# Performance work log

Hardware: AMD Instinct MI355X
Metric: run time of the kernel (lower is better)

Reference implementation:

```python
import jax, jax.numpy as jnp
import numpy as np

DIM, HEADS, DH, P, C = 2048, 8, 256, 7, 128
NP = (56 // P) ** 2          # 64 patches
N = NP + 1 + NP              # 65 pos tokens concatenated with 64 patch tokens = 129
PATCH_FEAT = C * P * P       # 6272
LN_EPS = 1e-5


def patchify(x, p):
    # 'b c (h p1) (w p2) -> b (h w) (p1 p2 c)'
    b, c, H, W = x.shape
    h, w = H // p, W // p
    x = x.reshape(b, c, h, p, w, p).transpose(0, 2, 4, 3, 5, 1)
    return x.reshape(b, h * w, p * p * c)


def setup_inputs() -> dict:
    key = jax.random.key(0)
    ks = jax.random.split(key, 16)
    s = 0.02
    d = dict(
        x_q=jax.random.normal(ks[0], (64, C, 56, 56), jnp.float32),
        x_kv=jax.random.normal(ks[1], (64, C, 56, 56), jnp.float32),
        W_ex=jax.random.normal(ks[2], (PATCH_FEAT, DIM), jnp.float32) * s,
        b_ex=jnp.zeros((DIM,), jnp.float32),
        W_en=jax.random.normal(ks[3], (PATCH_FEAT, DIM), jnp.float32) * s,
        b_en=jnp.zeros((DIM,), jnp.float32),
        pos=jax.random.normal(ks[4], (1, NP + 1, DIM), jnp.float32),
        Wq=jax.random.normal(ks[5], (DIM, HEADS * DH), jnp.float32) * s,
        Wk=jax.random.normal(ks[6], (DIM, HEADS * DH), jnp.float32) * s,
        Wv=jax.random.normal(ks[7], (DIM, HEADS * DH), jnp.float32) * s,
        Wo=jax.random.normal(ks[8], (HEADS * DH, DIM), jnp.float32) * s,
        bo=jnp.zeros((DIM,), jnp.float32),
        gamma=jnp.ones((DIM,), jnp.float32),
        beta=jnp.zeros((DIM,), jnp.float32),
        Wh=jax.random.normal(ks[9], (DIM, PATCH_FEAT), jnp.float32) * s,
        bh=jnp.zeros((PATCH_FEAT,), jnp.float32),
        Wm=jax.random.normal(ks[10], (DH, N), jnp.float32) * s,
        bm=jnp.zeros((N,), jnp.float32),
    )
    return d


def reference(x_q, x_kv, W_ex, b_ex, W_en, b_en, pos, Wq, Wk, Wv, Wo, bo,
              gamma, beta, Wh, bh, Wm, bm):
    b = x_q.shape[0]
    scale = DH ** -0.5
    # image embedder: patch embed + concat pos tokens
    tq = patchify(x_q, P) @ W_ex + b_ex                      # [b, 64, DIM]
    tk = patchify(x_kv, P) @ W_en + b_en                     # [b, 64, DIM]
    posb = jnp.broadcast_to(pos, (b, NP + 1, DIM))
    tq = jnp.concatenate([posb, tq], axis=1)                 # [b, N, DIM]
    tk = jnp.concatenate([posb, tk], axis=1)                 # [b, N, DIM]

    def split_heads(t):
        return t.reshape(b, N, HEADS, DH).transpose(0, 2, 1, 3)  # b h n d

    q = split_heads(tq @ Wq)
    k = split_heads(tk @ Wk)
    v = split_heads(tk @ Wv)

    # VAE-style reparameterize: mu=k, logvar=q
    eps = jax.random.normal(jax.random.key(42), k.shape, k.dtype)
    z = k + jnp.exp(0.5 * q) * eps                           # [b, h, n, d]

    # scale + linear remap d -> N, softmax, weighted sum with v
    dots = (z * scale) @ Wm + bm                             # [b, h, n, N]
    attn = jax.nn.softmax(dots, axis=-1)
    out = jnp.einsum('bhij,bhjd->bhid', attn, v)             # [b, h, n, d]
    out = out.transpose(0, 2, 1, 3).reshape(b, N, HEADS * DH)
    out = out @ Wo + bo                                      # [b, N, DIM]

    # mlp head: LayerNorm + Linear (final rearrange-to-image is shape-only, omitted)
    mu = out.mean(-1, keepdims=True)
    var = ((out - mu) ** 2).mean(-1, keepdims=True)
    ln = (out - mu) * jax.lax.rsqrt(var + LN_EPS) * gamma + beta
    head = ln @ Wh + bh                                      # [b, N, 6272]

    qf = q.reshape(b, -1)
    kf = k.reshape(b, -1)
    qn = qf / jnp.linalg.norm(qf, axis=1, keepdims=True)
    kn = kf / jnp.linalg.norm(kf, axis=1, keepdims=True)
    return head, qn, kn
```

## Files before the change

### kernel.cpp

```cpp
#include <hip/hip_runtime.h>


typedef unsigned short u16;
typedef short bf16x8 __attribute__((ext_vector_type(8)));
typedef unsigned short u16x8 __attribute__((ext_vector_type(8)));
typedef float f32x4 __attribute__((ext_vector_type(4)));

#define WAITV(N) asm volatile("s_waitcnt vmcnt(" #N ")" ::: "memory")

static __device__ __forceinline__ void barx() {
    asm volatile("" ::: "memory");
    __builtin_amdgcn_s_barrier();
    asm volatile("" ::: "memory");
}

static __device__ __forceinline__ u16 f2b(float f) {
    union { float f; unsigned int u; } cv; cv.f = f;
    unsigned int u = cv.u;
    unsigned int lsb = (u >> 16) & 1u;
    u += 0x7fffu + lsb;
    return (u16)(u >> 16);
}

static __device__ __forceinline__ float b2f(u16 u) {
    union { unsigned int i; float f; } c; c.i = ((unsigned int)u) << 16; return c.f;
}

static __device__ __forceinline__ void gemm8p_body(
    const u16* __restrict__ A, const u16* __restrict__ Bt, void* __restrict__ Cv,
    const float* __restrict__ bias, int M, int N, int K,
    int lda, int ldb, int ldc, float alpha, int c_bf16, int row_remap,
    int m0, int n0, u16* lds)
{
    const int tid = threadIdx.x, lane = tid & 63, wave = tid >> 6;
    const int wm = wave >> 2, wn = wave & 3;
    const int l15 = lane & 15, l4 = lane >> 4;
    const int scol = (((lane & 3) ^ ((lane >> 3) & 3)) << 3);
    const int bswz = ((l4 ^ ((l15 >> 1) & 3)) << 3);

    f32x4 acc[8][4] = {};
    const int nt = K >> 6;
    const int niter = nt >> 1;

    auto STAGE = [&](int tt, int kh, int isB) {
        const int c = tt & 1;
        const int k0 = (tt << 6) + (kh << 5);
        const int rbase = isB ? n0 : m0;
        const u16* P = isB ? Bt : A;
        const int ld = isB ? ldb : lda;
        const int lim = isB ? N : M;
        const int dbase = c * 32768 + isB * 16384 + kh * 8192;
        #pragma unroll
        for (int j = 0; j < 2; ++j) {
            const int r0 = j * 128 + wave * 16;
            int g = rbase + r0 + (lane >> 2); g = g < lim ? g : lim - 1;
            const u16* src = P + (long)g * ld + k0 + scol;
            __builtin_amdgcn_global_load_lds(
                (const __attribute__((address_space(1))) void*)src,
                (__attribute__((address_space(3))) void*)&lds[dbase + r0 * 32],
                16, 0, 0);
        }
    };

    bf16x8 bfr[4];
    auto LOADB = [&](int c, int kk) {
        #pragma unroll
        for (int nn = 0; nn < 4; ++nn) {
            const int row = wn * 64 + nn * 16 + l15;
            bfr[nn] = *(const bf16x8*)&lds[c * 32768 + 16384 + kk * 8192 + row * 32 + bswz];
        }
    };
    auto COMP = [&](int c, int kk, int mh) {
        bf16x8 af[4];
        #pragma unroll
        for (int mm = 0; mm < 4; ++mm) {
            const int row = wm * 128 + mh * 64 + mm * 16 + l15;
            af[mm] = *(const bf16x8*)&lds[c * 32768 + kk * 8192 + row * 32 + bswz];
        }
        __builtin_amdgcn_s_setprio(1);
        #pragma unroll
        for (int mm = 0; mm < 4; ++mm)
            #pragma unroll
            for (int nn = 0; nn < 4; ++nn)
                acc[mh * 4 + mm][nn] = __builtin_amdgcn_mfma_f32_16x16x32_bf16(
                    af[mm], bfr[nn], acc[mh * 4 + mm][nn], 0, 0, 0);
        __builtin_amdgcn_s_setprio(0);
    };

    STAGE(0, 0, 0); STAGE(0, 0, 1); STAGE(0, 1, 0); STAGE(0, 1, 1);
    STAGE(1, 0, 0); STAGE(1, 0, 1);

    for (int i = 0; i < niter; ++i) {
        const int t0 = 2 * i, t1 = t0 + 1;
        const bool has2 = (t0 + 2 < nt);
        STAGE(t1, 1, 0); WAITV(8);
        barx(); LOADB(0, 0); COMP(0, 0, 0); barx();
        STAGE(t1, 1, 1);
        barx(); COMP(0, 0, 1); barx();
        if (has2) STAGE(t0 + 2, 0, 0);
        WAITV(8);
        barx(); LOADB(0, 1); COMP(0, 1, 0); barx();
        if (has2) STAGE(t0 + 2, 0, 1);
        barx(); COMP(0, 1, 1); barx();
        if (has2) { STAGE(t0 + 2, 1, 0); WAITV(8); } else { WAITV(4); }
        barx(); LOADB(1, 0); COMP(1, 0, 0); barx();
        if (has2) STAGE(t0 + 2, 1, 1);
        barx(); COMP(1, 0, 1); barx();
        if (has2) { STAGE(t1 + 2, 0, 0); WAITV(8); } else { WAITV(0); }
        barx(); LOADB(1, 1); COMP(1, 1, 0); barx();
        if (has2) STAGE(t1 + 2, 0, 1);
        barx(); COMP(1, 1, 1); barx();
    }

    #pragma unroll
    for (int mr = 0; mr < 8; ++mr) {
        #pragma unroll
        for (int nn = 0; nn < 4; ++nn) {
            const int col = n0 + wn * 64 + nn * 16 + l15;
            if (col >= N) continue;
            const float bv = bias ? bias[col] : 0.0f;
            #pragma unroll
            for (int jj = 0; jj < 4; ++jj) {
                const int row = m0 + wm * 128 + mr * 16 + l4 * 4 + jj;
                if (row >= M) continue;
                float v = alpha * acc[mr][nn][jj] + bv;
                long crow = row;
                if (row_remap) crow = (long)(row >> 6) * 129 + 65 + (row & 63);
                if (c_bf16) ((u16*)Cv)[crow * (long)ldc + col] = f2b(v);
                else        ((float*)Cv)[crow * (long)ldc + col] = v;
            }
        }
    }
}

static __device__ __forceinline__ void xcd_swz(int& bx, int& by) {
    const int nbx = gridDim.x, nwg = nbx * gridDim.y;
    const int orig = blockIdx.y * nbx + blockIdx.x;
    const int q8 = nwg >> 3, r8 = nwg & 7;
    const int xcd = orig & 7, sidx = orig >> 3;
    const int wgid = (xcd < r8 ? xcd * (q8 + 1) : r8 * (q8 + 1) + (xcd - r8) * q8) + sidx;
    bx = wgid % nbx; by = wgid / nbx;
}

__global__ __launch_bounds__(512, 2) void gemm_8p(
    const u16* __restrict__ A, const u16* __restrict__ Bt, void* __restrict__ Cv,
    const float* __restrict__ bias, int M, int N, int K,
    int lda, int ldb, int ldc, float alpha, int c_bf16, int row_remap)
{
    __shared__ u16 lds[65536];
    int bx, by; xcd_swz(bx, by);
    gemm8p_body(A, Bt, Cv, bias, M, N, K, lda, ldb, ldc, alpha, c_bf16, row_remap,
                bx * 256, by * 256, lds);
}

__global__ __launch_bounds__(512, 2) void gemm_8p3(
    const u16* A0, const u16* A1, const u16* A2,
    const u16* B0, const u16* B1, const u16* B2,
    u16* C0, u16* C1, u16* C2,
    const float* bias0, const float* bias1, const float* bias2,
    int M, int N, int K, int lda, int ldb, int ldc, float alpha, int row_remap)
{
    __shared__ u16 lds[65536];
    int bx, by; xcd_swz(bx, by);
    const int z = blockIdx.z;
    const u16* A = z == 0 ? A0 : (z == 1 ? A1 : A2);
    const u16* B = z == 0 ? B0 : (z == 1 ? B1 : B2);
    u16* C = z == 0 ? C0 : (z == 1 ? C1 : C2);
    const float* bias = z == 0 ? bias0 : (z == 1 ? bias1 : bias2);
    gemm8p_body(A, B, C, bias, M, N, K, lda, ldb, ldc, alpha, 1, row_remap,
                bx * 256, by * 256, lds);
}

__global__ __launch_bounds__(256, 2) void gemm_pipe(
    const u16* __restrict__ A, const u16* __restrict__ Bt, void* __restrict__ Cv,
    const float* __restrict__ bias, int M, int N, int K,
    int lda, int ldb, int ldc, float alpha, int c_bf16, int row_remap)
{
    __shared__ u16 lds[2 * 16384];

    int bx, by; xcd_swz(bx, by);
    const int m0 = bx * 128, n0 = by * 128;

    const int tid = threadIdx.x, lane = tid & 63, wave = tid >> 6;
    const int wm = wave >> 1, wn = wave & 1;
    const int l15 = lane & 15, l4 = lane >> 4;

    const int srow = tid >> 3;
    const int scol = (((tid & 7) * 16) ^ (((tid >> 3) & 7) << 4)) >> 1;
    const int cf0 = (((0 * 64) + l4 * 16) ^ ((l15 & 7) << 4)) >> 1;
    const int cf1 = (((1 * 64) + l4 * 16) ^ ((l15 & 7) << 4)) >> 1;

    f32x4 acc[4][4] = {};
    const int nt = K >> 6;

    auto STAGE = [&](int c, int t) {
        const int k0 = t << 6;
        #pragma unroll
        for (int j = 0; j < 4; ++j) {
            const int r = j * 32 + srow;
            int ga = m0 + r; ga = ga < M ? ga : M - 1;
            const u16* srcA = A + (long)ga * lda + k0 + scol;
            __builtin_amdgcn_global_load_lds(
                (const __attribute__((address_space(1))) void*)srcA,
                (__attribute__((address_space(3))) void*)&lds[c * 16384 + j * 2048 + wave * 512],
                16, 0, 0);
            int gb = n0 + r; gb = gb < N ? gb : N - 1;
            const u16* srcB = Bt + (long)gb * ldb + k0 + scol;
            __builtin_amdgcn_global_load_lds(
                (const __attribute__((address_space(1))) void*)srcB,
                (__attribute__((address_space(3))) void*)&lds[c * 16384 + 8192 + j * 2048 + wave * 512],
                16, 0, 0);
        }
    };

    STAGE(0, 0);
    __syncthreads();
    for (int t = 0; t < nt; ++t) {
        const int c = t & 1;
        if (t + 1 < nt) STAGE(c ^ 1, t + 1);
        const int ab = c * 16384, bb = ab + 8192;
        #pragma unroll
        for (int kk = 0; kk < 2; ++kk) {
            const int cf = kk ? cf1 : cf0;
            bf16x8 af[4], bfr[4];
            #pragma unroll
            for (int m = 0; m < 4; ++m)
                af[m] = *(const bf16x8*)&lds[ab + (wm * 64 + m * 16 + l15) * 64 + cf];
            #pragma unroll
            for (int n = 0; n < 4; ++n)
                bfr[n] = *(const bf16x8*)&lds[bb + (wn * 64 + n * 16 + l15) * 64 + cf];
            __builtin_amdgcn_s_setprio(1);
            #pragma unroll
            for (int m = 0; m < 4; ++m)
                #pragma unroll
                for (int n = 0; n < 4; ++n)
                    acc[m][n] = __builtin_amdgcn_mfma_f32_16x16x32_bf16(
                        af[m], bfr[n], acc[m][n], 0, 0, 0);
            __builtin_amdgcn_s_setprio(0);
        }
        __syncthreads();
    }

    #pragma unroll
    for (int m = 0; m < 4; ++m) {
        #pragma unroll
        for (int n = 0; n < 4; ++n) {
            const int col = n0 + wn * 64 + n * 16 + l15;
            if (col >= N) continue;
            const float bv = bias ? bias[col] : 0.0f;
            #pragma unroll
            for (int j = 0; j < 4; ++j) {
                const int row = m0 + wm * 64 + m * 16 + l4 * 4 + j;
                if (row >= M) continue;
                float v = alpha * acc[m][n][j] + bv;
                long crow = row;
                if (row_remap) crow = (long)(row >> 6) * 129 + 65 + (row & 63);
                if (c_bf16) ((u16*)Cv)[crow * (long)ldc + col] = f2b(v);
                else        ((float*)Cv)[crow * (long)ldc + col] = v;
            }
        }
    }
}

__global__ __launch_bounds__(256) void gemm_bt(
    const u16* __restrict__ A, const u16* __restrict__ Bt, void* __restrict__ Cv,
    const float* __restrict__ bias, int M, int N, int K,
    int lda, int ldb, int ldc, float alpha, int c_bf16, int row_remap,
    long sA, long sB, long sCo, long sCi, int binner)
{
    const int bz = blockIdx.z;
    const u16* Ab = A + (long)bz * sA;
    const u16* Bb = Bt + (long)bz * sB;
    const long cOff = (long)(bz / binner) * sCo + (long)(bz % binner) * sCi;

    __shared__ u16 As[128][72];
    __shared__ u16 Bs[128][72];

    const int tid = threadIdx.x;
    const int lane = tid & 63;
    const int wave = tid >> 6;
    const int wr = wave >> 1, wc = wave & 1;
    const int l15 = lane & 15, l4 = lane >> 4;
    const int m0 = blockIdx.x * 128, n0 = blockIdx.y * 128;

    const int r = tid >> 3;
    const int kof = (tid & 7) * 8;

    f32x4 acc[4][4] = {};

    const int ktiles = (K + 63) / 64;
    for (int kt = 0; kt < ktiles; ++kt) {
        const int k0 = kt * 64;
        __syncthreads();
        #pragma unroll
        for (int i = 0; i < 4; ++i) {
            const int row = r + 32 * i;
            const int gk = k0 + kof;
            u16x8 v = {0,0,0,0,0,0,0,0};
            const int grow = m0 + row;
            if (grow < M && gk < K)
                v = *(const u16x8*)(Ab + (long)grow * lda + gk);
            *(u16x8*)&As[row][kof] = v;
        }
        #pragma unroll
        for (int i = 0; i < 4; ++i) {
            const int row = r + 32 * i;
            const int gk = k0 + kof;
            u16x8 v = {0,0,0,0,0,0,0,0};
            const int gcol = n0 + row;
            if (gcol < N && gk < K)
                v = *(const u16x8*)(Bb + (long)gcol * ldb + gk);
            *(u16x8*)&Bs[row][kof] = v;
        }
        __syncthreads();
        #pragma unroll
        for (int ks = 0; ks < 2; ++ks) {
            bf16x8 af[4], bfr[4];
            #pragma unroll
            for (int m = 0; m < 4; ++m)
                af[m] = *(const bf16x8*)&As[wr*64 + m*16 + l15][ks*32 + l4*8];
            #pragma unroll
            for (int n = 0; n < 4; ++n)
                bfr[n] = *(const bf16x8*)&Bs[wc*64 + n*16 + l15][ks*32 + l4*8];
            #pragma unroll
            for (int m = 0; m < 4; ++m)
                #pragma unroll
                for (int n = 0; n < 4; ++n)
                    acc[m][n] = __builtin_amdgcn_mfma_f32_16x16x32_bf16(
                        af[m], bfr[n], acc[m][n], 0, 0, 0);
        }
    }

    #pragma unroll
    for (int m = 0; m < 4; ++m) {
        #pragma unroll
        for (int n = 0; n < 4; ++n) {
            const int col = n0 + wc*64 + n*16 + l15;
            if (col >= N) continue;
            const float bv = bias ? bias[col] : 0.0f;
            #pragma unroll
            for (int j = 0; j < 4; ++j) {
                const int row = m0 + wr*64 + m*16 + l4*4 + j;
                if (row >= M) continue;
                float v = alpha * acc[m][n][j] + bv;
                long crow = row;
                if (row_remap) crow = (long)(row >> 6) * 129 + 65 + (row & 63);
                if (c_bf16) ((u16*)Cv)[cOff + crow * (long)ldc + col] = f2b(v);
                else        ((float*)Cv)[cOff + crow * (long)ldc + col] = v;
            }
        }
    }
}

__global__ __launch_bounds__(256) void transpose_conv(
    const float* __restrict__ in, u16* __restrict__ out, int K, int N, int KP, int NPd)
{
    __shared__ float tile[32][33];
    const int k0 = blockIdx.x * 32, n0 = blockIdx.y * 32;
    const int tx = threadIdx.x, ty = threadIdx.y;
    #pragma unroll
    for (int i = 0; i < 4; ++i) {
        const int k = k0 + ty + i*8, n = n0 + tx;
        tile[ty + i*8][tx] = (k < K && n < N) ? in[(long)k * N + n] : 0.0f;
    }
    __syncthreads();
    #pragma unroll
    for (int i = 0; i < 4; ++i) {
        const int n = n0 + ty + i*8, k = k0 + tx;
        if (n < NPd && k < KP) out[(long)n * KP + k] = f2b(tile[tx][ty + i*8]);
    }
}

__global__ __launch_bounds__(256) void patchify_kernel(
    const float* __restrict__ x, u16* __restrict__ out)
{
    __shared__ u16 tile[64 * 7 * 58];
    const int b = blockIdx.z, hh = blockIdx.y, cg = blockIdx.x;
    const int c0 = cg * 64;
    for (int i = threadIdx.x; i < 64 * 392; i += 256) {
        const int c = i / 392, rem = i - c * 392;
        const int p1 = rem / 56, w = rem - p1 * 56;
        const float v = x[(((long)b * 128 + c0 + c) * 56 + hh * 7 + p1) * 56 + w];
        tile[(c * 7 + p1) * 58 + w] = f2b(v);
    }
    __syncthreads();
    #pragma unroll
    for (int ww = 0; ww < 8; ++ww) {
        const long base = ((long)(b * 64 + hh * 8 + ww)) * 6272 + c0;
        for (int j = threadIdx.x; j < 49 * 64; j += 256) {
            const int c = j & 63, pp = j >> 6;
            const int p1 = pp / 7, p2 = pp - p1 * 7;
            out[base + pp * 128 + c] = tile[(c * 7 + p1) * 58 + ww * 7 + p2];
        }
    }
}

__global__ __launch_bounds__(256) void posfill_kernel(
    const float* __restrict__ pos, u16* __restrict__ Tq, u16* __restrict__ Tk)
{
    const int col = blockIdx.x * 256 + threadIdx.x;
    const int t = blockIdx.y, b = blockIdx.z;
    const u16 v = f2b(pos[(long)t * 2048 + col]);
    const long idx = ((long)b * 129 + t) * 2048 + col;
    Tq[idx] = v; Tk[idx] = v;
}

__global__ void vtrans_kernel(const u16* __restrict__ vmat, u16* __restrict__ v_t)
{
    const int bh = blockIdx.z; const int b = bh >> 3, h = bh & 7;
    const int d0 = blockIdx.x * 32, n0 = blockIdx.y * 32;
    __shared__ u16 tile[32][33];
    const int tx = threadIdx.x, ty = threadIdx.y;
    #pragma unroll
    for (int i = 0; i < 4; ++i) {
        const int n = n0 + ty + i*8;
        if (n < 129)
            tile[ty + i*8][tx] = vmat[((long)b*129 + n) * 2048 + h*256 + d0 + tx];
    }
    __syncthreads();
    #pragma unroll
    for (int i = 0; i < 4; ++i) {
        const int d = d0 + ty + i*8, n = n0 + tx;
        if (n < 144)
            v_t[((long)bh * 256 + d) * 144 + n] = (n < 129) ? tile[tx][ty + i*8] : (u16)0;
    }
}

static __device__ __forceinline__ unsigned int rotl32(unsigned int x, int d) {
    return (x << d) | (x >> (32 - d));
}

static __device__ __forceinline__ float threefry_normal(unsigned int i) {
    const unsigned int ks0 = 0u, ks1 = 42u;
    const unsigned int ks2 = ks0 ^ ks1 ^ 0x1BD11BDAu;
    unsigned int x0 = 0u + ks0;
    unsigned int x1 = i + ks1;
#define TF_R(rr) { x0 += x1; x1 = rotl32(x1, rr); x1 ^= x0; }
    TF_R(13) TF_R(15) TF_R(26) TF_R(6)
    x0 += ks1; x1 += ks2 + 1u;
    TF_R(17) TF_R(29) TF_R(16) TF_R(24)
    x0 += ks2; x1 += ks0 + 2u;
    TF_R(13) TF_R(15) TF_R(26) TF_R(6)
    x0 += ks0; x1 += ks1 + 3u;
    TF_R(17) TF_R(29) TF_R(16) TF_R(24)
    x0 += ks1; x1 += ks2 + 4u;
    TF_R(13) TF_R(15) TF_R(26) TF_R(6)
    x0 += ks2; x1 += ks0 + 5u;
#undef TF_R
    const unsigned int bits = x0 ^ x1;
    const unsigned int fb = (bits >> 9) | 0x3f800000u;
    union { unsigned int u; float f; } cv; cv.u = fb;
    const float f = cv.f - 1.0f;
    const float lo = -0.99999994f;
    float u = f * (1.0f - lo) + lo;
    u = fmaxf(lo, u);
    return 1.4142135623730951f * erfinvf(u);
}

__global__ __launch_bounds__(256) void z_kernel(
    const u16* __restrict__ qmat, const u16* __restrict__ kmat,
    const float* __restrict__ norms, u16* __restrict__ z,
    float* __restrict__ outq, float* __restrict__ outk)
{
    const unsigned int i = blockIdx.x * 256u + threadIdx.x;
    const int d = i & 255; const unsigned int t = i >> 8;
    const int n = t % 129; const int bh = t / 129;
    const int b = bh >> 3, h = bh & 7;
    const long src = ((long)(b * 129 + n)) * 2048 + h * 256 + d;
    const float qf = b2f(qmat[src]);
    const float kf = b2f(kmat[src]);
    const float eps = threefry_normal(i);
    z[i] = f2b(kf + expf(0.5f * qf) * eps);
    outq[i] = qf / norms[b];
    outk[i] = kf / norms[64 + b];
}

__global__ __launch_bounds__(256) void softmax_kernel(
    const float* __restrict__ dots, u16* __restrict__ attn)
{
    const int row = blockIdx.x * 4 + (threadIdx.x >> 6);
    const int lane = threadIdx.x & 63;
    const float* dr = dots + (long)row * 144;
    const float v0 = dr[lane];
    const float v1 = dr[64 + lane];
    const float v2 = (lane == 0) ? dr[128] : -1e30f;
    float m = fmaxf(fmaxf(v0, v1), v2);
    #pragma unroll
    for (int o = 32; o > 0; o >>= 1) m = fmaxf(m, __shfl_xor(m, o, 64));
    const float e0 = expf(v0 - m), e1 = expf(v1 - m);
    const float e2 = (lane == 0) ? expf(v2 - m) : 0.0f;
    float s = e0 + e1 + e2;
    #pragma unroll
    for (int o = 32; o > 0; o >>= 1) s += __shfl_xor(s, o, 64);
    const float inv = 1.0f / s;
    u16* ar = attn + (long)row * 144;
    ar[lane] = f2b(e0 * inv);
    ar[64 + lane] = f2b(e1 * inv);
    if (lane < 16) ar[128 + lane] = (lane == 0) ? f2b(e2 * inv) : (u16)0;
}

__global__ __launch_bounds__(256) void ln_kernel(
    const float* __restrict__ proj, const float* __restrict__ gamma,
    const float* __restrict__ beta, u16* __restrict__ ln)
{
    const int row = blockIdx.x;
    const float* p = proj + (long)row * 2048;
    const int tid = threadIdx.x;
    float v[8]; float s = 0.f, s2 = 0.f;
    #pragma unroll
    for (int i = 0; i < 8; ++i) {
        v[i] = p[tid + i * 256]; s += v[i]; s2 += v[i] * v[i];
    }
    #pragma unroll
    for (int o = 32; o > 0; o >>= 1) { s += __shfl_down(s, o, 64); s2 += __shfl_down(s2, o, 64); }
    __shared__ float sh[8];
    if ((tid & 63) == 0) { sh[tid >> 6] = s; sh[4 + (tid >> 6)] = s2; }
    __syncthreads();
    s = sh[0] + sh[1] + sh[2] + sh[3];
    s2 = sh[4] + sh[5] + sh[6] + sh[7];
    const float mu = s * (1.0f / 2048.0f);
    const float var = s2 * (1.0f / 2048.0f) - mu * mu;
    const float rinv = 1.0f / sqrtf(var + 1e-5f);
    u16* lr = ln + (long)row * 2048;
    #pragma unroll
    for (int i = 0; i < 8; ++i) {
        const int c = tid + i * 256;
        lr[c] = f2b((v[i] - mu) * rinv * gamma[c] + beta[c]);
    }
}

__global__ __launch_bounds__(256) void norm_reduce(
    const u16* __restrict__ qmat, const u16* __restrict__ kmat, float* __restrict__ norms)
{
    const int b = blockIdx.x & 63;
    const u16* src = (blockIdx.x >= 64 ? kmat : qmat) + (long)b * 264192;
    float s = 0.f;
    for (int i = threadIdx.x; i < 264192; i += 256) { const float x = b2f(src[i]); s += x * x; }
    #pragma unroll
    for (int o = 32; o > 0; o >>= 1) s += __shfl_down(s, o, 64);
    __shared__ float sh[4];
    if ((threadIdx.x & 63) == 0) sh[threadIdx.x >> 6] = s;
    __syncthreads();
    if (threadIdx.x == 0) norms[blockIdx.x] = sqrtf(sh[0] + sh[1] + sh[2] + sh[3]);
}

extern "C" void kernel_launch(void* const* d_in, const int* in_sizes, int n_in,
                              void* d_out, int out_size, void* d_ws, size_t ws_size,
                              hipStream_t stream)
{
    const float* x_q   = (const float*)d_in[0];
    const float* x_kv  = (const float*)d_in[1];
    const float* W_ex  = (const float*)d_in[2];
    const float* b_ex  = (const float*)d_in[3];
    const float* W_en  = (const float*)d_in[4];
    const float* b_en  = (const float*)d_in[5];
    const float* pos   = (const float*)d_in[6];
    const float* Wq    = (const float*)d_in[7];
    const float* Wk    = (const float*)d_in[8];
    const float* Wv    = (const float*)d_in[9];
    const float* Wo    = (const float*)d_in[10];
    const float* bo    = (const float*)d_in[11];
    const float* gamma = (const float*)d_in[12];
    const float* beta  = (const float*)d_in[13];
    const float* Wh    = (const float*)d_in[14];
    const float* bh    = (const float*)d_in[15];
    const float* Wm    = (const float*)d_in[16];
    const float* bm    = (const float*)d_in[17];
    (void)in_sizes; (void)n_in; (void)out_size; (void)ws_size;

    char* ws = (char*)d_ws;
    size_t off = 0;
    auto alloc = [&](size_t bytes) -> char* {
        char* p = ws + off;
        off += (bytes + 255) & ~(size_t)255;
        return p;
    };
    u16*   Xq_p  = (u16*)alloc(4096UL * 6272 * 2);
    u16*   Xk_p  = (u16*)alloc(4096UL * 6272 * 2);
    u16*   Wex_t = (u16*)alloc(2048UL * 6272 * 2);
    u16*   Wen_t = (u16*)alloc(2048UL * 6272 * 2);
    u16*   Tq    = (u16*)alloc(8256UL * 2048 * 2);
    u16*   Tk    = (u16*)alloc(8256UL * 2048 * 2);
    u16*   Wq_t  = (u16*)alloc(2048UL * 2048 * 2);
    u16*   Wk_t  = (u16*)alloc(2048UL * 2048 * 2);
    u16*   Wv_t  = (u16*)alloc(2048UL * 2048 * 2);
    u16*   qmat  = (u16*)alloc(8256UL * 2048 * 2);
    u16*   kmat  = (u16*)alloc(8256UL * 2048 * 2);
    u16*   vmat  = (u16*)alloc(8256UL * 2048 * 2);
    u16*   v_t   = (u16*)alloc(512UL * 256 * 144 * 2);
    u16*   z     = (u16*)alloc(66048UL * 256 * 2);
    float* dots  = (float*)alloc(66048UL * 144 * 4);
    u16*   attn  = (u16*)alloc(66048UL * 144 * 2);
    u16*   outm  = (u16*)alloc(8256UL * 2048 * 2);
    float* proj  = (float*)alloc(8256UL * 2048 * 4);
    u16*   ln    = (u16*)alloc(8256UL * 2048 * 2);
    u16*   Wo_t  = (u16*)alloc(2048UL * 2048 * 2);
    u16*   Wh_t  = (u16*)alloc(6272UL * 2048 * 2);
    u16*   Wm_t  = (u16*)alloc(144UL * 256 * 2);
    float* norms = (float*)alloc(128UL * 4);

    auto tconv = [&](const float* in, u16* out, int K, int N, int KP, int NPd) {
        dim3 grid((KP + 31) / 32, (NPd + 31) / 32);
        transpose_conv<<<grid, dim3(32, 8), 0, stream>>>(in, out, K, N, KP, NPd);
    };
    auto slow_gemm = [&](const u16* A, const u16* Bt, void* C, const float* bias,
                         int M, int N, int K, int lda, int ldb, int ldc,
                         float alpha, int cbf16, int remap, int batch,
                         long sA, long sB, long sCo, long sCi, int binner) {
        dim3 grid((M + 127) / 128, (N + 127) / 128, batch);
        gemm_bt<<<grid, 256, 0, stream>>>(A, Bt, C, bias, M, N, K, lda, ldb, ldc,
                                          alpha, cbf16, remap, sA, sB, sCo, sCi, binner);
    };

    tconv(W_ex, Wex_t, 6272, 2048, 6272, 2048);
    tconv(W_en, Wen_t, 6272, 2048, 6272, 2048);
    patchify_kernel<<<dim3(2, 8, 64), 256, 0, stream>>>(x_q, Xq_p);
    patchify_kernel<<<dim3(2, 8, 64), 256, 0, stream>>>(x_kv, Xk_p);
    posfill_kernel<<<dim3(8, 65, 64), 256, 0, stream>>>(pos, Tq, Tk);

    gemm_8p3<<<dim3(16, 8, 2), 512, 0, stream>>>(
        Xq_p, Xk_p, Xk_p, Wex_t, Wen_t, Wen_t, Tq, Tk, Tk,
        b_ex, b_en, b_en, 4096, 2048, 6272, 6272, 6272, 2048, 1.0f, 1);

    tconv(Wq, Wq_t, 2048, 2048, 2048, 2048);
    tconv(Wk, Wk_t, 2048, 2048, 2048, 2048);
    tconv(Wv, Wv_t, 2048, 2048, 2048, 2048);
    gemm_8p3<<<dim3(33, 8, 3), 512, 0, stream>>>(
        Tq, Tk, Tk, Wq_t, Wk_t, Wv_t, qmat, kmat, vmat,
        nullptr, nullptr, nullptr, 8256, 2048, 2048, 2048, 2048, 2048, 1.0f, 0);

    vtrans_kernel<<<dim3(8, 5, 512), dim3(32, 8), 0, stream>>>(vmat, v_t);

    norm_reduce<<<128, 256, 0, stream>>>(qmat, kmat, norms);
    {
        float* outq = (float*)d_out + 51781632L;
        float* outk = outq + 16908288L;
        z_kernel<<<66048, 256, 0, stream>>>(qmat, kmat, norms, z, outq, outk);
    }

    tconv(Wm, Wm_t, 256, 129, 256, 144);
    slow_gemm(z, Wm_t, dots, bm, 66048, 129, 256, 256, 256, 144,
              0.0625f, 0, 0, 1, 0, 0, 0, 0, 1);

    softmax_kernel<<<16512, 256, 0, stream>>>(dots, attn);

    slow_gemm(attn, v_t, outm, nullptr, 129, 256, 144, 144, 144, 2048,
              1.0f, 1, 0, 512, 129L * 144, 256L * 144, 129L * 2048, 256L, 8);

    tconv(Wo, Wo_t, 2048, 2048, 2048, 2048);
    gemm_pipe<<<dim3(65, 16), 256, 0, stream>>>(
        outm, Wo_t, proj, bo, 8256, 2048, 2048, 2048, 2048, 2048, 1.0f, 0, 0);

    ln_kernel<<<8256, 256, 0, stream>>>(proj, gamma, beta, ln);

    tconv(Wh, Wh_t, 2048, 6272, 2048, 6272);
    gemm_8p<<<dim3(33, 25), 512, 0, stream>>>(
        ln, Wh_t, (float*)d_out, bh, 8256, 6272, 2048, 2048, 2048, 6272, 1.0f, 0, 0);
}
```

Measured before the change: 1.687 ms.

## Fuse dots GEMM with softmax, batch transposes, split attn-V tail row

Replaces the generic dots GEMM plus separate softmax with one MFMA kernel that holds Wm in LDS and does the softmax in registers, so the fp32 dots buffer never goes to memory. It merges the weight-transpose and patchify launches into multi-input kernels to cut launch count. The attention-times-V GEMM now covers only 128 rows, and a small kernel handles row 128 so the extra M tile is not wasted. The main GEMM loop also splits the A-fragment loads from the MFMAs so the second half's LDS reads are issued early. Padding columns 129-143 of attn are written as zeros, and both the fdots grid and row128 assume fixed shapes.

```diff
diff --git a/kernel.cpp b/kernel.cpp
--- a/kernel.cpp
+++ b/kernel.cpp
@@ -70,13 +70,14 @@
             bfr[nn] = *(const bf16x8*)&lds[c * 32768 + 16384 + kk * 8192 + row * 32 + bswz];
         }
     };
-    auto COMP = [&](int c, int kk, int mh) {
-        bf16x8 af[4];
+    auto LDA = [&](int c, int kk, int mh, bf16x8* af) {
         #pragma unroll
         for (int mm = 0; mm < 4; ++mm) {
             const int row = wm * 128 + mh * 64 + mm * 16 + l15;
             af[mm] = *(const bf16x8*)&lds[c * 32768 + kk * 8192 + row * 32 + bswz];
         }
+    };
+    auto MM = [&](const bf16x8* af, int mh) {
         __builtin_amdgcn_s_setprio(1);
         #pragma unroll
         for (int mm = 0; mm < 4; ++mm)
@@ -90,26 +91,27 @@
     STAGE(0, 0, 0); STAGE(0, 0, 1); STAGE(0, 1, 0); STAGE(0, 1, 1);
     STAGE(1, 0, 0); STAGE(1, 0, 1);
 
+    bf16x8 a0[4], a1[4];
     for (int i = 0; i < niter; ++i) {
         const int t0 = 2 * i, t1 = t0 + 1;
         const bool has2 = (t0 + 2 < nt);
         STAGE(t1, 1, 0); WAITV(8);
-        barx(); LOADB(0, 0); COMP(0, 0, 0); barx();
+        barx(); LOADB(0, 0); LDA(0, 0, 0, a0); MM(a0, 0); LDA(0, 0, 1, a1); barx();
         STAGE(t1, 1, 1);
-        barx(); COMP(0, 0, 1); barx();
+        barx(); MM(a1, 1); barx();
         if (has2) STAGE(t0 + 2, 0, 0);
         WAITV(8);
-        barx(); LOADB(0, 1); COMP(0, 1, 0); barx();
+        barx(); LOADB(0, 1); LDA(0, 1, 0, a0); MM(a0, 0); LDA(0, 1, 1, a1); barx();
         if (has2) STAGE(t0 + 2, 0, 1);
-        barx(); COMP(0, 1, 1); barx();
+        barx(); MM(a1, 1); barx();
         if (has2) { STAGE(t0 + 2, 1, 0); WAITV(8); } else { WAITV(4); }
-        barx(); LOADB(1, 0); COMP(1, 0, 0); barx();
+        barx(); LOADB(1, 0); LDA(1, 0, 0, a0); MM(a0, 0); LDA(1, 0, 1, a1); barx();
         if (has2) STAGE(t0 + 2, 1, 1);
-        barx(); COMP(1, 0, 1); barx();
+        barx(); MM(a1, 1); barx();
         if (has2) { STAGE(t1 + 2, 0, 0); WAITV(8); } else { WAITV(0); }
-        barx(); LOADB(1, 1); COMP(1, 1, 0); barx();
+        barx(); LOADB(1, 1); LDA(1, 1, 0, a0); MM(a0, 0); LDA(1, 1, 1, a1); barx();
         if (has2) STAGE(t1 + 2, 0, 1);
-        barx(); COMP(1, 1, 1); barx();
+        barx(); MM(a1, 1); barx();
     }
 
     #pragma unroll
@@ -352,9 +354,101 @@
     }
 }
 
-__global__ __launch_bounds__(256) void transpose_conv(
-    const float* __restrict__ in, u16* __restrict__ out, int K, int N, int KP, int NPd)
-{
+__global__ __launch_bounds__(256, 2) void fdots_kernel(
+    const u16* __restrict__ z, const u16* __restrict__ Wm_t,
+    const float* __restrict__ bm, u16* __restrict__ attn)
+{
+    __shared__ u16 wlds[144 * 264];
+    const int tid = threadIdx.x;
+    for (int i = tid; i < 144 * 32; i += 256) {
+        const int row = i >> 5, c8 = i & 31;
+        *(u16x8*)&wlds[row * 264 + c8 * 8] = *(const u16x8*)&Wm_t[row * 256 + c8 * 8];
+    }
+    __syncthreads();
+    const int lane = tid & 63, wave = tid >> 6;
+    const int l15 = lane & 15, l4 = lane >> 4;
+    const long rowbase = (long)blockIdx.x * 128 + wave * 32;
+
+    f32x4 acc[2][9] = {};
+    #pragma unroll
+    for (int kk = 0; kk < 8; ++kk) {
+        bf16x8 af[2];
+        #pragma unroll
+        for (int rg = 0; rg < 2; ++rg)
+            af[rg] = *(const bf16x8*)&z[(rowbase + rg * 16 + l15) * 256 + kk * 32 + l4 * 8];
+        #pragma unroll
+        for (int c = 0; c < 9; ++c) {
+            const bf16x8 bf = *(const bf16x8*)&wlds[(c * 16 + l15) * 264 + kk * 32 + l4 * 8];
+            #pragma unroll
+            for (int rg = 0; rg < 2; ++rg)
+                acc[rg][c] = __builtin_amdgcn_mfma_f32_16x16x32_bf16(af[rg], bf, acc[rg][c], 0, 0, 0);
+        }
+    }
+
+    float bmv[9];
+    #pragma unroll
+    for (int c = 0; c < 9; ++c) {
+        const int col = c * 16 + l15;
+        bmv[c] = (col < 129) ? bm[col] : 0.0f;
+    }
+
+    #pragma unroll
+    for (int rg = 0; rg < 2; ++rg) {
+        #pragma unroll
+        for (int j = 0; j < 4; ++j) {
+            float v[9]; float mx = -1e30f;
+            #pragma unroll
+            for (int c = 0; c < 9; ++c) {
+                const int col = c * 16 + l15;
+                v[c] = (col < 129) ? (0.0625f * acc[rg][c][j] + bmv[c]) : -1e30f;
+                mx = fmaxf(mx, v[c]);
+            }
+            #pragma unroll
+            for (int o = 1; o < 16; o <<= 1) mx = fmaxf(mx, __shfl_xor(mx, o, 64));
+            float s = 0.f;
+            #pragma unroll
+            for (int c = 0; c < 9; ++c) {
+                v[c] = (c * 16 + l15 < 129) ? expf(v[c] - mx) : 0.0f;
+                s += v[c];
+            }
+            #pragma unroll
+            for (int o = 1; o < 16; o <<= 1) s += __shfl_xor(s, o, 64);
+            const float inv = 1.0f / s;
+            u16* ar = attn + (rowbase + rg * 16 + l4 * 4 + j) * 144;
+            #pragma unroll
+            for (int c = 0; c < 9; ++c)
+                ar[c * 16 + l15] = f2b(v[c] * inv);
+        }
+    }
+}
+
+__global__ __launch_bounds__(256) void row128_kernel(
+    const u16* __restrict__ attn, const u16* __restrict__ v_t, u16* __restrict__ outm)
+{
+    const int bh = blockIdx.x, d = threadIdx.x;
+    const int b = bh >> 3, h = bh & 7;
+    __shared__ float a[144];
+    for (int j = threadIdx.x; j < 144; j += 256)
+        a[j] = (j < 129) ? b2f(attn[((long)bh * 129 + 128) * 144 + j]) : 0.0f;
+    __syncthreads();
+    const u16* vr = v_t + ((long)bh * 256 + d) * 144;
+    float s = 0.f;
+    #pragma unroll
+    for (int j8 = 0; j8 < 18; ++j8) {
+        const bf16x8 vv = *(const bf16x8*)&vr[j8 * 8];
+        #pragma unroll
+        for (int e = 0; e < 8; ++e) s += a[j8 * 8 + e] * b2f((u16)vv[e]);
+    }
+    outm[((long)(b * 129 + 128)) * 2048 + h * 256 + d] = f2b(s);
+}
+
+__global__ __launch_bounds__(256) void transpose_conv4(
+    const float* in0, const float* in1, const float* in2, const float* in3,
+    u16* o0, u16* o1, u16* o2, u16* o3, int K, int N, int KP, int NPd)
+{
+    const int zz = blockIdx.z;
+    const float* in = zz == 0 ? in0 : (zz == 1 ? in1 : (zz == 2 ? in2 : in3));
+    u16* out = zz == 0 ? o0 : (zz == 1 ? o1 : (zz == 2 ? o2 : o3));
     __shared__ float tile[32][33];
     const int k0 = blockIdx.x * 32, n0 = blockIdx.y * 32;
     const int tx = threadIdx.x, ty = threadIdx.y;
@@ -372,10 +466,14 @@
 }
 
 __global__ __launch_bounds__(256) void patchify_kernel(
-    const float* __restrict__ x, u16* __restrict__ out)
+    const float* __restrict__ xq, const float* __restrict__ xkv,
+    u16* __restrict__ oq, u16* __restrict__ okv)
 {
     __shared__ u16 tile[64 * 7 * 58];
-    const int b = blockIdx.z, hh = blockIdx.y, cg = blockIdx.x;
+    const int zz = blockIdx.z;
+    const float* x = (zz >= 64) ? xkv : xq;
+    u16* out = (zz >= 64) ? okv : oq;
+    const int b = zz & 63, hh = blockIdx.y, cg = blockIdx.x;
     const int c0 = cg * 64;
     for (int i = threadIdx.x; i < 64 * 392; i += 256) {
         const int c = i / 392, rem = i - c * 392;
@@ -475,30 +573,6 @@
     outk[i] = kf / norms[64 + b];
 }
 
-__global__ __launch_bounds__(256) void softmax_kernel(
-    const float* __restrict__ dots, u16* __restrict__ attn)
-{
-    const int row = blockIdx.x * 4 + (threadIdx.x >> 6);
-    const int lane = threadIdx.x & 63;
-    const float* dr = dots + (long)row * 144;
-    const float v0 = dr[lane];
-    const float v1 = dr[64 + lane];
-    const float v2 = (lane == 0) ? dr[128] : -1e30f;
-    float m = fmaxf(fmaxf(v0, v1), v2);
-    #pragma unroll
-    for (int o = 32; o > 0; o >>= 1) m = fmaxf(m, __shfl_xor(m, o, 64));
-    const float e0 = expf(v0 - m), e1 = expf(v1 - m);
-    const float e2 = (lane == 0) ? expf(v2 - m) : 0.0f;
-    float s = e0 + e1 + e2;
-    #pragma unroll
-    for (int o = 32; o > 0; o >>= 1) s += __shfl_xor(s, o, 64);
-    const float inv = 1.0f / s;
-    u16* ar = attn + (long)row * 144;
-    ar[lane] = f2b(e0 * inv);
-    ar[64 + lane] = f2b(e1 * inv);
-    if (lane < 16) ar[128 + lane] = (lane == 0) ? f2b(e2 * inv) : (u16)0;
-}
-
 __global__ __launch_bounds__(256) void ln_kernel(
     const float* __restrict__ proj, const float* __restrict__ gamma,
     const float* __restrict__ beta, u16* __restrict__ ln)
@@ -589,7 +663,6 @@
     u16*   vmat  = (u16*)alloc(8256UL * 2048 * 2);
     u16*   v_t   = (u16*)alloc(512UL * 256 * 144 * 2);
     u16*   z     = (u16*)alloc(66048UL * 256 * 2);
-    float* dots  = (float*)alloc(66048UL * 144 * 4);
     u16*   attn  = (u16*)alloc(66048UL * 144 * 2);
     u16*   outm  = (u16*)alloc(8256UL * 2048 * 2);
     float* proj  = (float*)alloc(8256UL * 2048 * 4);
@@ -599,32 +672,17 @@
     u16*   Wm_t  = (u16*)alloc(144UL * 256 * 2);
     float* norms = (float*)alloc(128UL * 4);
 
-    auto tconv = [&](const float* in, u16* out, int K, int N, int KP, int NPd) {
-        dim3 grid((KP + 31) / 32, (NPd + 31) / 32);
-        transpose_conv<<<grid, dim3(32, 8), 0, stream>>>(in, out, K, N, KP, NPd);
-    };
-    auto slow_gemm = [&](const u16* A, const u16* Bt, void* C, const float* bias,
-                         int M, int N, int K, int lda, int ldb, int ldc,
-                         float alpha, int cbf16, int remap, int batch,
-                         long sA, long sB, long sCo, long sCi, int binner) {
-        dim3 grid((M + 127) / 128, (N + 127) / 128, batch);
-        gemm_bt<<<grid, 256, 0, stream>>>(A, Bt, C, bias, M, N, K, lda, ldb, ldc,
-                                          alpha, cbf16, remap, sA, sB, sCo, sCi, binner);
-    };
-
-    tconv(W_ex, Wex_t, 6272, 2048, 6272, 2048);
-    tconv(W_en, Wen_t, 6272, 2048, 6272, 2048);
-    patchify_kernel<<<dim3(2, 8, 64), 256, 0, stream>>>(x_q, Xq_p);
-    patchify_kernel<<<dim3(2, 8, 64), 256, 0, stream>>>(x_kv, Xk_p);
+    transpose_conv4<<<dim3(196, 64, 2), dim3(32, 8), 0, stream>>>(
+        W_ex, W_en, W_ex, W_en, Wex_t, Wen_t, Wex_t, Wen_t, 6272, 2048, 6272, 2048);
+    patchify_kernel<<<dim3(2, 8, 128), 256, 0, stream>>>(x_q, x_kv, Xq_p, Xk_p);
     posfill_kernel<<<dim3(8, 65, 64), 256, 0, stream>>>(pos, Tq, Tk);
 
     gemm_8p3<<<dim3(16, 8, 2), 512, 0, stream>>>(
         Xq_p, Xk_p, Xk_p, Wex_t, Wen_t, Wen_t, Tq, Tk, Tk,
         b_ex, b_en, b_en, 4096, 2048, 6272, 6272, 6272, 2048, 1.0f, 1);
 
-    tconv(Wq, Wq_t, 2048, 2048, 2048, 2048);
-    tconv(Wk, Wk_t, 2048, 2048, 2048, 2048);
-    tconv(Wv, Wv_t, 2048, 2048, 2048, 2048);
+    transpose_conv4<<<dim3(64, 64, 4), dim3(32, 8), 0, stream>>>(
+        Wq, Wk, Wv, Wo, Wq_t, Wk_t, Wv_t, Wo_t, 2048, 2048, 2048, 2048);
     gemm_8p3<<<dim3(33, 8, 3), 512, 0, stream>>>(
         Tq, Tk, Tk, Wq_t, Wk_t, Wv_t, qmat, kmat, vmat,
         nullptr, nullptr, nullptr, 8256, 2048, 2048, 2048, 2048, 2048, 1.0f, 0);
@@ -638,22 +696,25 @@
         z_kernel<<<66048, 256, 0, stream>>>(qmat, kmat, norms, z, outq, outk);
     }
 
-    tconv(Wm, Wm_t, 256, 129, 256, 144);
-    slow_gemm(z, Wm_t, dots, bm, 66048, 129, 256, 256, 256, 144,
-              0.0625f, 0, 0, 1, 0, 0, 0, 0, 1);
-
-    softmax_kernel<<<16512, 256, 0, stream>>>(dots, attn);
-
-    slow_gemm(attn, v_t, outm, nullptr, 129, 256, 144, 144, 144, 2048,
-              1.0f, 1, 0, 512, 129L * 144, 256L * 144, 129L * 2048, 256L, 8);
-
-    tconv(Wo, Wo_t, 2048, 2048, 2048, 2048);
+    transpose_conv4<<<dim3(8, 5, 1), dim3(32, 8), 0, stream>>>(
+        Wm, Wm, Wm, Wm, Wm_t, Wm_t, Wm_t, Wm_t, 256, 129, 256, 144);
+    fdots_kernel<<<516, 256, 0, stream>>>(z, Wm_t, bm, attn);
+
+    {
+        dim3 grid(1, 2, 512);
+        gemm_bt<<<grid, 256, 0, stream>>>(attn, v_t, outm, nullptr,
+            128, 256, 144, 144, 144, 2048, 1.0f, 1, 0,
+            129L * 144, 256L * 144, 129L * 2048, 256L, 8);
+    }
+    row128_kernel<<<512, 256, 0, stream>>>(attn, v_t, outm);
+
     gemm_pipe<<<dim3(65, 16), 256, 0, stream>>>(
         outm, Wo_t, proj, bo, 8256, 2048, 2048, 2048, 2048, 2048, 1.0f, 0, 0);
 
     ln_kernel<<<8256, 256, 0, stream>>>(proj, gamma, beta, ln);
 
-    tconv(Wh, Wh_t, 2048, 6272, 2048, 6272);
+    transpose_conv4<<<dim3(64, 196, 1), dim3(32, 8), 0, stream>>>(
+        Wh, Wh, Wh, Wh, Wh_t, Wh_t, Wh_t, Wh_t, 2048, 6272, 2048, 6272);
     gemm_8p<<<dim3(33, 25), 512, 0, stream>>>(
         ln, Wh_t, (float*)d_out, bh, 8256, 6272, 2048, 2048, 2048, 6272, 1.0f, 0, 0);
 }
```

New measurement: 1.628 ms. 1.04x faster.
